# Kernel optimization log

Hardware: AMD Instinct MI355X
Metric: run time of the kernel (lower is better)

Reference implementation:

```python
import jax, jax.numpy as jnp
import numpy as np

# near_sym_b (13,19)-tap biorthogonal level-1 DTCWT filters (Kingsbury)
H0O = np.array([-0.0017578125, 0.0, 0.022265625, -0.046875, -0.0482421875,
                0.296875, 0.5554687500, 0.296875, -0.0482421875, -0.046875,
                0.022265625, 0.0, -0.0017578125], dtype=np.float32)
H1O = np.array([-7.0626e-05, 0.0, 1.34189e-03, -1.88341e-03, -7.15660e-03,
                2.38560e-02, 5.56431e-02, -5.16881e-02, -2.99758e-01,
                5.59431e-01, -2.99758e-01, -5.16881e-02, 5.56431e-02,
                2.38560e-02, -7.15660e-03, -1.88341e-03, 1.34189e-03,
                0.0, -7.0626e-05], dtype=np.float32)

def _alt(h):
    c = (len(h) - 1) // 2
    return (h * ((-1.0) ** (np.arange(len(h)) - c))).astype(np.float32)

G0O = _alt(H1O)  # synthesis lowpass  (PR complement of H1O)
G1O = _alt(H0O)  # synthesis highpass (PR complement of H0O)

DIM, HS, WS, BATCH, NB, BS = 64, 56, 56, 32, 4, 16


def _filt(x, h, axis):
    # depthwise 1D correlation with symmetric padding; x: (B,C,H,W), axis in {2,3}
    L = len(h); p = L // 2
    pad = [(0, 0)] * 4; pad[axis] = (p, p)
    xp = jnp.pad(x, pad, mode='symmetric')
    k = jnp.asarray(h, x.dtype).reshape((1, 1, L, 1) if axis == 2 else (1, 1, 1, L))
    B, C = x.shape[:2]
    y = jax.lax.conv_general_dilated(
        xp.reshape((B * C, 1) + xp.shape[2:]), k, (1, 1), 'VALID',
        dimension_numbers=('NCHW', 'OIHW', 'NCHW'))
    return y.reshape((B, C) + y.shape[2:])


def _q2c(y):
    y = y * np.float32(1.0 / np.sqrt(2.0))
    a = y[..., 0::2, 0::2]; b = y[..., 0::2, 1::2]
    c = y[..., 1::2, 0::2]; d = y[..., 1::2, 1::2]
    return (a - d, b + c), (a + d, b - c)


def _c2q(w1r, w1i, w2r, w2i):
    sc = np.float32(1.0 / np.sqrt(2.0))
    B, C, Hh, Wh = w1r.shape
    top = jnp.stack([(w1r + w2r) * sc, (w1i + w2i) * sc], axis=-1).reshape(B, C, Hh, 2 * Wh)
    bot = jnp.stack([(w1i - w2i) * sc, (w2r - w1r) * sc], axis=-1).reshape(B, C, Hh, 2 * Wh)
    return jnp.stack([top, bot], axis=3).reshape(B, C, 2 * Hh, 2 * Wh)


def dtcwt_fwd_j1(x):
    lo = _filt(x, H0O, 3); hi = _filt(x, H1O, 3)
    ll = _filt(lo, H0O, 2)
    (d15r, d15i), (d165r, d165i) = _q2c(_filt(lo, H1O, 2))   # LH -> 15/165 deg
    (d75r, d75i), (d105r, d105i) = _q2c(_filt(hi, H0O, 2))   # HL -> 75/105 deg
    (d45r, d45i), (d135r, d135i) = _q2c(_filt(hi, H1O, 2))   # HH -> 45/135 deg
    real = jnp.stack([d15r, d45r, d75r, d105r, d135r, d165r], axis=2)
    imag = jnp.stack([d15i, d45i, d75i, d105i, d135i, d165i], axis=2)
    return ll, jnp.stack([real, imag], axis=-1)  # (B,C,H,W), (B,C,6,H/2,W/2,2)


def dtcwt_inv_j1(ll, yh):
    r = yh[..., 0]; im = yh[..., 1]
    lh = _c2q(r[:, :, 0], im[:, :, 0], r[:, :, 5], im[:, :, 5])
    hl = _c2q(r[:, :, 2], im[:, :, 2], r[:, :, 3], im[:, :, 3])
    hh = _c2q(r[:, :, 1], im[:, :, 1], r[:, :, 4], im[:, :, 4])
    lo = _filt(ll, G0O, 2) + _filt(lh, G1O, 2)
    hi = _filt(hl, G0O, 2) + _filt(hh, G1O, 2)
    return _filt(lo, G0O, 3) + _filt(hi, G1O, 3)


def setup_inputs():
    key = jax.random.key(0)
    ks = jax.random.split(key, 6)
    return {
        'x': jax.random.normal(ks[0], (BATCH, HS * WS, DIM), jnp.float32),
        'w_ll': jax.random.normal(ks[1], (DIM, HS, WS), jnp.float32) * 0.02,
        'w1': jax.random.normal(ks[2], (2, NB, BS, BS), jnp.float32) * 0.02,
        'w2': jax.random.normal(ks[3], (2, NB, BS, BS), jnp.float32) * 0.02,
        'b1': jax.random.normal(ks[4], (2, NB, BS), jnp.float32) * 0.02,
        'b2': jax.random.normal(ks[5], (2, NB, BS), jnp.float32) * 0.02,
        'H': HS, 'W': WS,
    }


def reference(x, w_ll, w1, w2, b1, b2, H, W):
    Bt, N, C = x.shape
    xi = jnp.transpose(x.reshape(Bt, H, W, C), (0, 3, 1, 2)).astype(jnp.float32)
    xl, xh = dtcwt_fwd_j1(xi)
    xl = xl * w_ll                                  # (B,C,H,W) * (C,H,W)
    Hh, Wh = H // 2, W // 2
    # (B,C,6,Hh,Wh,2) -> (2,B,6,Hh,Wh,C) -> split C into (NB,BS) blocks
    xh = jnp.transpose(xh, (5, 0, 2, 3, 4, 1)).reshape(2, Bt, 6, Hh, Wh, NB, BS)
    xr, xim = xh[0], xh[1]
    mul = lambda t, w: jnp.einsum('...bd,bdk->...bk', t, w)
    r1 = jax.nn.relu(mul(xr, w1[0]) - mul(xim, w1[1]) + b1[0])
    i1 = jax.nn.relu(mul(xr, w1[1]) + mul(xim, w1[0]) + b1[1])
    r2 = mul(r1, w2[0]) - mul(i1, w2[1]) + b2[0]
    i2 = mul(r1, w2[1]) + mul(i1, w2[0]) + b2[1]
    xh2 = jnp.stack([r2, i2], axis=-1).reshape(Bt, 6, Hh, Wh, C, 2)
    xh2 = jnp.transpose(xh2, (0, 4, 1, 2, 3, 5))    # (B,C,6,Hh,Wh,2)
    y = dtcwt_inv_j1(xl, xh2)
    return jnp.transpose(y, (0, 2, 3, 1)).reshape(Bt, N, C)
```

## Files before the change

kernel.cpp:

```cpp
#include <hip/hip_runtime.h>

#define BT 32
#define CH 64
#define HS 56
#define WS 56
#define HH 28
#define WH 28

namespace {
constexpr float ISQ2 = 0.70710678118654752440f;
constexpr float F_H0[13] = {-0.0017578125f, 0.0f, 0.022265625f, -0.046875f,
    -0.0482421875f, 0.296875f, 0.55546875f, 0.296875f, -0.0482421875f,
    -0.046875f, 0.022265625f, 0.0f, -0.0017578125f};
constexpr float F_H1[19] = {-7.0626e-05f, 0.0f, 0.00134189f, -0.00188341f,
    -0.0071566f, 0.023856f, 0.0556431f, -0.0516881f, -0.299758f, 0.559431f,
    -0.299758f, -0.0516881f, 0.0556431f, 0.023856f, -0.0071566f,
    -0.00188341f, 0.00134189f, 0.0f, -7.0626e-05f};
constexpr float F_G0[19] = {7.0626e-05f, 0.0f, -0.00134189f, -0.00188341f,
    0.0071566f, 0.023856f, -0.0556431f, -0.0516881f, 0.299758f, 0.559431f,
    0.299758f, -0.0516881f, -0.0556431f, 0.023856f, 0.0071566f,
    -0.00188341f, -0.00134189f, 0.0f, 7.0626e-05f};
constexpr float F_G1[13] = {-0.0017578125f, 0.0f, 0.022265625f, 0.046875f,
    -0.0482421875f, -0.296875f, 0.55546875f, -0.296875f, -0.0482421875f,
    0.046875f, 0.022265625f, 0.0f, -0.0017578125f};
}

__device__ __forceinline__ int symi(int k) {
    k = (k < 0) ? (-1 - k) : k;
    k = (k >= HS) ? (2 * HS - 1 - k) : k;
    return k;
}

__device__ __forceinline__ unsigned short f2bf(float f) {
    unsigned u = __float_as_uint(f);
    u += 0x7fffu + ((u >> 16) & 1u);
    return (unsigned short)(u >> 16);
}
__device__ __forceinline__ float bf2f(unsigned short h) {
    return __uint_as_float(((unsigned)h) << 16);
}
__device__ __forceinline__ float2 bfp2(unsigned u) {
    float2 r;
    r.x = __uint_as_float((u & 0xffffu) << 16);
    r.y = __uint_as_float(u & 0xffff0000u);
    return r;
}
__device__ __forceinline__ unsigned packbf(float a, float b) {
    return (unsigned)f2bf(a) | ((unsigned)f2bf(b) << 16);
}

typedef __attribute__((ext_vector_type(8))) short short8;
typedef __attribute__((ext_vector_type(4))) float f32x4;

#define PPOS 784

__global__ __launch_bounds__(256) void k_fwd_rows(const float* __restrict__ x,
                                                  unsigned short* __restrict__ lo,
                                                  unsigned short* __restrict__ hi,
                                                  const float* __restrict__ wll,
                                                  float* __restrict__ wllT) {
    int b = blockIdx.x / HS, h = blockIdx.x % HS;
    int strip = threadIdx.x >> 5;
    int c0 = (threadIdx.x & 31) * 2;
    int base = (b * HS + h) * WS * CH + c0;
    const float* row = x + base;
    unsigned short* lop = lo + base;
    unsigned short* hip = hi + base;
    int w0s = strip * 7;
    float Wa[19], Wb[19];
#pragma unroll
    for (int t = 0; t < 19; ++t) {
        float2 v = *(const float2*)(row + symi(w0s - 9 + t) * CH);
        Wa[t] = v.x; Wb[t] = v.y;
    }
    float2 nW[7];
#pragma unroll
    for (int u = 0; u < 7; ++u) nW[u] = *(const float2*)(row + symi(w0s + u + 10) * CH);
#pragma unroll
    for (int u = 0; u < 7; ++u) {
        int w = w0s + u;
        float aLo = 0.f, aHi = 0.f, bLo = 0.f, bHi = 0.f;
#pragma unroll
        for (int t = 0; t < 13; ++t) { aLo += F_H0[t] * Wa[3 + t]; bLo += F_H0[t] * Wb[3 + t]; }
#pragma unroll
        for (int t = 0; t < 19; ++t) { aHi += F_H1[t] * Wa[t]; bHi += F_H1[t] * Wb[t]; }
        *(unsigned*)(lop + w * CH) = packbf(aLo, bLo);
        *(unsigned*)(hip + w * CH) = packbf(aHi, bHi);
#pragma unroll
        for (int t = 0; t < 18; ++t) { Wa[t] = Wa[t + 1]; Wb[t] = Wb[t + 1]; }
        Wa[18] = nW[u].x; Wb[18] = nW[u].y;
    }
    if (blockIdx.x < 49) {
        __shared__ float tile[64][65];
        int pos0 = blockIdx.x * 64;
        int lp = threadIdx.x & 63, g = threadIdx.x >> 6;
#pragma unroll
        for (int r = 0; r < 16; ++r) {
            int cc = r * 4 + g;
            tile[cc][lp] = wll[cc * (HS * WS) + pos0 + lp];
        }
        __syncthreads();
#pragma unroll
        for (int r = 0; r < 16; ++r) {
            int pl = r * 4 + g;
            wllT[(pos0 + pl) * CH + lp] = tile[lp][pl];
        }
    }
}

__global__ __launch_bounds__(256) void k_cols_mix(
    const unsigned short* __restrict__ lo_in,
    const unsigned short* __restrict__ hi_in, const float* __restrict__ wllT,
    const float* __restrict__ w1, const float* __restrict__ w2,
    const float* __restrict__ b1, const float* __restrict__ b2,
    unsigned short* __restrict__ xl, unsigned short* __restrict__ P0,
    unsigned short* __restrict__ P1, unsigned short* __restrict__ P2) {
    __shared__ __align__(16) unsigned short qTb[2][4][14][64];
    __shared__ __align__(16) unsigned short pA[8][14][72];
    unsigned short (*l1a)[16][36] =
        reinterpret_cast<unsigned short(*)[16][36]>(&qTb[0][0][0][0]);
    unsigned short (*l1b)[16][36] = l1a + 4;

    int hf = blockIdx.y;
    int zmode = blockIdx.z;
    int b = blockIdx.x / WH, wp = blockIdx.x % WH;
    int w0 = 2 * wp, tid = threadIdx.x;
    int q = tid >> 6, c = tid & 63;
    int rp = q >> 1, jc = q & 1;
    const unsigned short* srcp = zmode ? hi_in : lo_in;
    const unsigned short* colbase = srcp + (b * HS) * WS * CH + (w0 + jc) * CH + c;
    {
        int hstart = 2 * (hf * 14) + rp;
        float W[19];
#pragma unroll
        for (int t = 0; t < 19; ++t) W[t] = bf2f(colbase[symi(hstart - 9 + t) * (WS * CH)]);
        for (int rnd = 0; rnd < 2; ++rnd) {
            float nW0[7], nW1[7], nwll[7];
            int ii0 = rnd * 7;
#pragma unroll
            for (int u = 0; u < 7; ++u) {
                int h = hstart + 2 * (ii0 + u);
                nW0[u] = bf2f(colbase[symi(h + 10) * (WS * CH)]);
                nW1[u] = bf2f(colbase[symi(h + 11) * (WS * CH)]);
            }
            if (zmode == 0) {
#pragma unroll
                for (int u = 0; u < 7; ++u)
                    nwll[u] = wllT[((hstart + 2 * (ii0 + u)) * WS + (w0 + jc)) * CH + c];
            }
#pragma unroll
            for (int u = 0; u < 7; ++u) {
                int ii = ii0 + u;
                int h = hstart + 2 * ii;
                float v0 = 0.f, v1 = 0.f;
#pragma unroll
                for (int t = 0; t < 13; ++t) v0 += F_H0[t] * W[3 + t];
#pragma unroll
                for (int t = 0; t < 19; ++t) v1 += F_H1[t] * W[t];
                if (zmode == 0) {
                    xl[((b * HS + h) * WS + (w0 + jc)) * CH + c] = f2bf(v0 * nwll[u]);
                    qTb[0][q][ii][c] = f2bf(v1);
                } else {
                    qTb[0][q][ii][c] = f2bf(v0);
                    qTb[1][q][ii][c] = f2bf(v1);
                }
#pragma unroll
                for (int t = 0; t < 17; ++t) W[t] = W[t + 2];
                W[17] = nW0[u];
                W[18] = nW1[u];
            }
        }
    }
    __syncthreads();
    {
        int qq = tid >> 5;
        int role = qq & 3, half = qq >> 2;
        int c0 = (tid & 31) * 2;
        int rowA = role & 1, rowB = 3 - (role & 1);
        float sgn = (role == 1 || role == 2) ? 1.f : -1.f;
        if (zmode == 0) {
#pragma unroll
            for (int g = 0; g < 7; ++g) {
                int ii = half * 7 + g;
                float2 av = bfp2(*(const unsigned*)&qTb[0][rowA][ii][c0]);
                float2 bv = bfp2(*(const unsigned*)&qTb[0][rowB][ii][c0]);
                float v0 = (av.x + sgn * bv.x) * ISQ2;
                float v1 = (av.y + sgn * bv.y) * ISQ2;
                *(unsigned*)&pA[role][ii][c0] = packbf(v0, v1);
            }
        } else {
#pragma unroll
            for (int src = 0; src < 2; ++src) {
                int pl = (src == 0) ? (2 + role) : ((role < 2) ? role : (4 + role));
#pragma unroll
                for (int g = 0; g < 7; ++g) {
                    int ii = half * 7 + g;
                    float2 av = bfp2(*(const unsigned*)&qTb[src][rowA][ii][c0]);
                    float2 bv = bfp2(*(const unsigned*)&qTb[src][rowB][ii][c0]);
                    float v0 = (av.x + sgn * bv.x) * ISQ2;
                    float v1 = (av.y + sgn * bv.y) * ISQ2;
                    *(unsigned*)&pA[pl][ii][c0] = packbf(v0, v1);
                }
            }
        }
    }
    __syncthreads();

    int lane = tid & 63;
    int wv = tid >> 6;
    int nb = __builtin_amdgcn_readfirstlane(wv);
    int quad = lane >> 4;
    int n = lane & 15;
    int rix = quad >> 1, dlo = (quad & 1) * 8;
    int chb = nb * 16 + dlo;
    int npos = (n < 14) ? n : 0;

    short8 B1r, B1i, B2r, B2i;
#pragma unroll
    for (int j = 0; j < 8; ++j) {
        int kk = quad * 8 + j;
        int riw = kk >> 4, dd = kk & 15;
        float v1r = w1[nb * 256 + dd * 16 + n];
        float v1i = w1[1024 + nb * 256 + dd * 16 + n];
        float v2r = w2[nb * 256 + dd * 16 + n];
        float v2i = w2[1024 + nb * 256 + dd * 16 + n];
        B1r[j] = (short)f2bf(riw ? -v1i : v1r);
        B1i[j] = (short)f2bf(riw ? v1r : v1i);
        B2r[j] = (short)f2bf(riw ? -v2i : v2r);
        B2i[j] = (short)f2bf(riw ? v2r : v2i);
    }
    float bias1r = b1[nb * 16 + n], bias1i = b1[64 + nb * 16 + n];
    float bias2r = b2[nb * 16 + n], bias2i = b2[64 + nb * 16 + n];

    auto mixprod = [&](int aP, int bP, unsigned short* __restrict__ Pd) {
        short8 A1a = *(const short8*)&pA[aP][npos][chb];
        short8 A1b = *(const short8*)&pA[bP][npos][chb];
        f32x4 a1r = {bias1r, bias1r, bias1r, bias1r};
        f32x4 a1i = {bias1i, bias1i, bias1i, bias1i};
        f32x4 b1r_ = a1r, b1i_ = a1i;
        a1r = __builtin_amdgcn_mfma_f32_16x16x32_bf16(A1a, B1r, a1r, 0, 0, 0);
        a1i = __builtin_amdgcn_mfma_f32_16x16x32_bf16(A1a, B1i, a1i, 0, 0, 0);
        b1r_ = __builtin_amdgcn_mfma_f32_16x16x32_bf16(A1b, B1r, b1r_, 0, 0, 0);
        b1i_ = __builtin_amdgcn_mfma_f32_16x16x32_bf16(A1b, B1i, b1i_, 0, 0, 0);
#pragma unroll
        for (int r = 0; r < 4; ++r) {
            int pos = quad * 4 + r;
            l1a[wv][pos][n] = f2bf(fmaxf(a1r[r], 0.f));
            l1a[wv][pos][16 + n] = f2bf(fmaxf(a1i[r], 0.f));
            l1b[wv][pos][n] = f2bf(fmaxf(b1r_[r], 0.f));
            l1b[wv][pos][16 + n] = f2bf(fmaxf(b1i_[r], 0.f));
        }
        union { short8 s8; uint2 u2[2]; } a2a, a2b;
        const unsigned short* rowpa = &l1a[wv][n][0];
        const unsigned short* rowpb = &l1b[wv][n][0];
        a2a.u2[0] = *(const uint2*)(rowpa + quad * 8);
        a2a.u2[1] = *(const uint2*)(rowpa + quad * 8 + 4);
        a2b.u2[0] = *(const uint2*)(rowpb + quad * 8);
        a2b.u2[1] = *(const uint2*)(rowpb + quad * 8 + 4);
        f32x4 aAr = {bias2r, bias2r, bias2r, bias2r};
        f32x4 aAi = {bias2i, bias2i, bias2i, bias2i};
        f32x4 aBr = aAr, aBi = aAi;
        aAr = __builtin_amdgcn_mfma_f32_16x16x32_bf16(a2a.s8, B2r, aAr, 0, 0, 0);
        aAi = __builtin_amdgcn_mfma_f32_16x16x32_bf16(a2a.s8, B2i, aAi, 0, 0, 0);
        aBr = __builtin_amdgcn_mfma_f32_16x16x32_bf16(a2b.s8, B2r, aBr, 0, 0, 0);
        aBi = __builtin_amdgcn_mfma_f32_16x16x32_bf16(a2b.s8, B2i, aBi, 0, 0, 0);
#pragma unroll
        for (int r = 0; r < 4; ++r) {
            int m = quad * 4 + r;
            if (m < 14) {
                int iig = hf * 14 + m;
                int o = ((b * HS + 2 * iig) * WS + 2 * wp) * CH + nb * 16 + n;
                Pd[o] = f2bf((aAr[r] + aBr[r]) * ISQ2);
                Pd[o + CH] = f2bf((aAi[r] + aBi[r]) * ISQ2);
                Pd[o + WS * CH] = f2bf((aAi[r] - aBi[r]) * ISQ2);
                Pd[o + WS * CH + CH] = f2bf((aBr[r] - aAr[r]) * ISQ2);
            }
        }
    };

    if (zmode == 0) {
        mixprod(rix, 2 + rix, P0);
    } else {
        mixprod(2 + rix, 4 + rix, P1);
        mixprod(rix, 6 + rix, P2);
    }
}

template <int MODE>
__device__ __forceinline__ void inv_cols_body(
    const unsigned short* __restrict__ xl, const unsigned short* __restrict__ P0,
    const unsigned short* __restrict__ P1, const unsigned short* __restrict__ P2,
    unsigned short* __restrict__ lo2, unsigned short* __restrict__ hi2) {
    int hf = blockIdx.y;
    int b = blockIdx.x / 7, wg = blockIdx.x % 7;
    int wl = threadIdx.x >> 5, l = threadIdx.x & 31;
    int c0 = l * 2;
    int w = wg * 8 + wl;
    int base = (b * HS) * WS * CH + w * CH + c0;
    const int st = WS * CH;
    const unsigned short* Ap = (MODE == 0) ? xl : P1;
    const unsigned short* Bp = (MODE == 0) ? P0 : P2;
    unsigned short* outp = (MODE == 0) ? lo2 : hi2;
    auto ldA = [&](int r) -> float2 {
        return bfp2(*(const unsigned*)(Ap + base + r * st));
    };
    auto ldB = [&](int r) -> float2 {
        return bfp2(*(const unsigned*)(Bp + base + r * st));
    };
    int h0 = hf * 14;
    float Aa[19], Ab[19], Ba[13], Bb[13];
#pragma unroll
    for (int t = 0; t < 19; ++t) { float2 v = ldA(symi(h0 - 9 + t)); Aa[t] = v.x; Ab[t] = v.y; }
#pragma unroll
    for (int t = 0; t < 13; ++t) { float2 v = ldB(symi(h0 - 6 + t)); Ba[t] = v.x; Bb[t] = v.y; }
    float2 pa0[4], pb0[4], pa1[4], pb1[4];
#define LDG(bA, bB, OFF, CNT)                                                   \
    {                                                                           \
        _Pragma("unroll") for (int u = 0; u < (CNT); ++u)                       \
            bA[u] = ldA(symi(h0 + (OFF) + u + 10));                             \
        _Pragma("unroll") for (int u = 0; u < (CNT); ++u)                       \
            bB[u] = ldB(symi(h0 + (OFF) + u + 7));                              \
    }
#define CPG(bA, bB, OFF, CNT)                                                   \
    {                                                                           \
        _Pragma("unroll") for (int u = 0; u < (CNT); ++u) {                     \
            int h = h0 + (OFF) + u;                                             \
            float acca = 0.f, accb = 0.f;                                       \
            _Pragma("unroll") for (int t = 0; t < 19; ++t) {                    \
                acca += F_G0[t] * Aa[t]; accb += F_G0[t] * Ab[t];               \
            }                                                                   \
            _Pragma("unroll") for (int t = 0; t < 13; ++t) {                    \
                acca += F_G1[t] * Ba[t]; accb += F_G1[t] * Bb[t];               \
            }                                                                   \
            *(unsigned*)(outp + base + h * st) = packbf(acca, accb);            \
            _Pragma("unroll") for (int t = 0; t < 18; ++t) {                    \
                Aa[t] = Aa[t + 1]; Ab[t] = Ab[t + 1];                           \
            }                                                                   \
            _Pragma("unroll") for (int t = 0; t < 12; ++t) {                    \
                Ba[t] = Ba[t + 1]; Bb[t] = Bb[t + 1];                           \
            }                                                                   \
            Aa[18] = bA[u].x; Ab[18] = bA[u].y;                                 \
            Ba[12] = bB[u].x; Bb[12] = bB[u].y;                                 \
        }                                                                       \
    }
    LDG(pa0, pb0, 0, 4) LDG(pa1, pb1, 4, 4)
    CPG(pa0, pb0, 0, 4) LDG(pa0, pb0, 8, 4)
    CPG(pa1, pb1, 4, 4) LDG(pa1, pb1, 12, 2)
    CPG(pa0, pb0, 8, 4)
    CPG(pa1, pb1, 12, 2)
#undef LDG
#undef CPG
}

__global__ __launch_bounds__(256) void k_inv_cols(
    const unsigned short* __restrict__ xl, const unsigned short* __restrict__ P0,
    const unsigned short* __restrict__ P1, const unsigned short* __restrict__ P2,
    unsigned short* __restrict__ lo2, unsigned short* __restrict__ hi2) {
    if (blockIdx.z == 0)
        inv_cols_body<0>(xl, P0, P1, P2, lo2, hi2);
    else
        inv_cols_body<1>(xl, P0, P1, P2, lo2, hi2);
}

__global__ __launch_bounds__(256) void k_inv_rows(
    const unsigned short* __restrict__ lo2,
    const unsigned short* __restrict__ hi2, float* __restrict__ out) {
    int b = blockIdx.x / HS, h = blockIdx.x % HS;
    int strip = threadIdx.x >> 5;
    int c0 = (threadIdx.x & 31) * 2;
    int base = (b * HS + h) * WS * CH + c0;
    const unsigned short* rlo = lo2 + base;
    const unsigned short* rhi = hi2 + base;
    float* op = out + base;
    int w0s = strip * 7;
    float Aa[19], Ab[19], Ba[13], Bb[13];
#pragma unroll
    for (int t = 0; t < 19; ++t) {
        float2 v = bfp2(*(const unsigned*)(rlo + symi(w0s - 9 + t) * CH));
        Aa[t] = v.x; Ab[t] = v.y;
    }
#pragma unroll
    for (int t = 0; t < 13; ++t) {
        float2 v = bfp2(*(const unsigned*)(rhi + symi(w0s - 6 + t) * CH));
        Ba[t] = v.x; Bb[t] = v.y;
    }
    float2 nA[7], nB[7];
#pragma unroll
    for (int u = 0; u < 7; ++u) nA[u] = bfp2(*(const unsigned*)(rlo + symi(w0s + u + 10) * CH));
#pragma unroll
    for (int u = 0; u < 7; ++u) nB[u] = bfp2(*(const unsigned*)(rhi + symi(w0s + u + 7) * CH));
#pragma unroll
    for (int u = 0; u < 7; ++u) {
        int w = w0s + u;
        float acca = 0.f, accb = 0.f;
#pragma unroll
        for (int t = 0; t < 19; ++t) { acca += F_G0[t] * Aa[t]; accb += F_G0[t] * Ab[t]; }
#pragma unroll
        for (int t = 0; t < 13; ++t) { acca += F_G1[t] * Ba[t]; accb += F_G1[t] * Bb[t]; }
        float2 ov; ov.x = acca; ov.y = accb;
        *(float2*)(op + w * CH) = ov;
#pragma unroll
        for (int t = 0; t < 18; ++t) { Aa[t] = Aa[t + 1]; Ab[t] = Ab[t + 1]; }
#pragma unroll
        for (int t = 0; t < 12; ++t) { Ba[t] = Ba[t + 1]; Bb[t] = Bb[t + 1]; }
        Aa[18] = nA[u].x; Ab[18] = nA[u].y;
        Ba[12] = nB[u].x; Bb[12] = nB[u].y;
    }
}

extern "C" void kernel_launch(void* const* d_in, const int* in_sizes, int n_in,
                              void* d_out, int out_size, void* d_ws, size_t ws_size,
                              hipStream_t stream) {
    const float* x = (const float*)d_in[0];
    const float* w_ll = (const float*)d_in[1];
    const float* w1 = (const float*)d_in[2];
    const float* w2 = (const float*)d_in[3];
    const float* b1 = (const float*)d_in[4];
    const float* b2 = (const float*)d_in[5];
    float* out = (float*)d_out;

    const size_t A = (size_t)BT * HS * WS * CH;
    const size_t SBf = (size_t)12 * 64 * BT * PPOS / 2;
    float* wsf = (float*)d_ws;
    unsigned short* xl = (unsigned short*)wsf;
    unsigned short* lo2 = (unsigned short*)(wsf + A);
    unsigned short* hi2 = (unsigned short*)(wsf + A + SBf);
    unsigned short* lo_in = (unsigned short*)(wsf + A + SBf + A);
    unsigned short* hi_in = lo_in + A;
    unsigned short* P0 = hi_in + A;
    unsigned short* P1 = P0 + A;
    unsigned short* P2 = P1 + A;

    float* wllT = out;

    k_fwd_rows<<<BT * HS, 256, 0, stream>>>(x, lo_in, hi_in, w_ll, wllT);
    k_cols_mix<<<dim3(BT * WH, 2, 2), 256, 0, stream>>>(lo_in, hi_in, wllT, w1,
                                                        w2, b1, b2, xl, P0, P1, P2);
    k_inv_cols<<<dim3(BT * 7, 4, 2), 256, 0, stream>>>(xl, P0, P1, P2, lo2, hi2);
    k_inv_rows<<<BT * HS, 256, 0, stream>>>(lo2, hi2, out);
}
```

Before: 162.8 us.

## Specialize cols_mix on mode/half, ring-buffer window, packed bf16 cvt, precompute weights

Templates the column/mix kernel on z-mode and half index so symmetric-boundary handling applies only on the side that needs it. It replaces the shifting filter window with an indexed ring buffer and uses v_cvt_pk_bf16_f32 for paired bf16 conversions. The bf16 MFMA weight fragments are now built once by a spare block of the forward-rows kernel and stored in a workspace slot, rather than recomputed in every cols_mix block. This trims address math, register moves and conversion instructions, at the cost of more code size and a dependency on the workspace layout.

```diff
diff --git a/kernel.cpp b/kernel.cpp
--- a/kernel.cpp
+++ b/kernel.cpp
@@ -30,6 +30,8 @@
     k = (k >= HS) ? (2 * HS - 1 - k) : k;
     return k;
 }
+__device__ __forceinline__ int symi_lo(int k) { return (k < 0) ? (-1 - k) : k; }
+__device__ __forceinline__ int symi_hi(int k) { return (k >= HS) ? (2 * HS - 1 - k) : k; }
 
 __device__ __forceinline__ unsigned short f2bf(float f) {
     unsigned u = __float_as_uint(f);
@@ -38,6 +40,11 @@
 }
 __device__ __forceinline__ float bf2f(unsigned short h) {
     return __uint_as_float(((unsigned)h) << 16);
+}
+__device__ __forceinline__ unsigned cvtpk(float lo, float hi) {
+    unsigned r;
+    asm("v_cvt_pk_bf16_f32 %0, %1, %2" : "=v"(r) : "v"(lo), "v"(hi));
+    return r;
 }
 __device__ __forceinline__ float2 bfp2(unsigned u) {
     float2 r;
@@ -58,7 +65,10 @@
                                                   unsigned short* __restrict__ lo,
                                                   unsigned short* __restrict__ hi,
                                                   const float* __restrict__ wll,
-                                                  float* __restrict__ wllT) {
+                                                  float* __restrict__ wllT,
+                                                  const float* __restrict__ w1,
+                                                  const float* __restrict__ w2,
+                                                  unsigned short* __restrict__ wB) {
     int b = blockIdx.x / HS, h = blockIdx.x % HS;
     int strip = threadIdx.x >> 5;
     int c0 = (threadIdx.x & 31) * 2;
@@ -105,69 +115,96 @@
             int pl = r * 4 + g;
             wllT[(pos0 + pl) * CH + lp] = tile[lp][pl];
         }
-    }
-}
-
-__global__ __launch_bounds__(256) void k_cols_mix(
+    } else if (blockIdx.x == 49) {
+        int tid = threadIdx.x;
+        int lane = tid & 63;
+        int nb = tid >> 6;
+        int quad = lane >> 4, n = lane & 15;
+        short8 B1r, B1i, B2r, B2i;
+#pragma unroll
+        for (int j = 0; j < 8; ++j) {
+            int kk = quad * 8 + j;
+            int riw = kk >> 4, dd = kk & 15;
+            float v1r = w1[nb * 256 + dd * 16 + n];
+            float v1i = w1[1024 + nb * 256 + dd * 16 + n];
+            float v2r = w2[nb * 256 + dd * 16 + n];
+            float v2i = w2[1024 + nb * 256 + dd * 16 + n];
+            B1r[j] = (short)f2bf(riw ? -v1i : v1r);
+            B1i[j] = (short)f2bf(riw ? v1r : v1i);
+            B2r[j] = (short)f2bf(riw ? -v2i : v2r);
+            B2i[j] = (short)f2bf(riw ? v2r : v2i);
+        }
+        *(short8*)(wB + (0 * 256 + tid) * 8) = B1r;
+        *(short8*)(wB + (1 * 256 + tid) * 8) = B1i;
+        *(short8*)(wB + (2 * 256 + tid) * 8) = B2r;
+        *(short8*)(wB + (3 * 256 + tid) * 8) = B2i;
+    }
+}
+
+template <int ZM, int HF>
+__device__ __forceinline__ void cols_mix_body(
+    unsigned short (&qTb)[2][4][14][64], unsigned short (&pA)[8][14][72],
     const unsigned short* __restrict__ lo_in,
     const unsigned short* __restrict__ hi_in, const float* __restrict__ wllT,
-    const float* __restrict__ w1, const float* __restrict__ w2,
-    const float* __restrict__ b1, const float* __restrict__ b2,
-    unsigned short* __restrict__ xl, unsigned short* __restrict__ P0,
-    unsigned short* __restrict__ P1, unsigned short* __restrict__ P2) {
-    __shared__ __align__(16) unsigned short qTb[2][4][14][64];
-    __shared__ __align__(16) unsigned short pA[8][14][72];
+    const unsigned short* __restrict__ wB, const float* __restrict__ b1,
+    const float* __restrict__ b2, unsigned short* __restrict__ xl,
+    unsigned short* __restrict__ P0, unsigned short* __restrict__ P1,
+    unsigned short* __restrict__ P2) {
     unsigned short (*l1a)[16][36] =
         reinterpret_cast<unsigned short(*)[16][36]>(&qTb[0][0][0][0]);
     unsigned short (*l1b)[16][36] = l1a + 4;
 
-    int hf = blockIdx.y;
-    int zmode = blockIdx.z;
     int b = blockIdx.x / WH, wp = blockIdx.x % WH;
     int w0 = 2 * wp, tid = threadIdx.x;
     int q = tid >> 6, c = tid & 63;
     int rp = q >> 1, jc = q & 1;
-    const unsigned short* srcp = zmode ? hi_in : lo_in;
+    const unsigned short* srcp = ZM ? hi_in : lo_in;
     const unsigned short* colbase = srcp + (b * HS) * WS * CH + (w0 + jc) * CH + c;
     {
-        int hstart = 2 * (hf * 14) + rp;
+        int hstart = HF * 28 + rp;
         float W[19];
 #pragma unroll
-        for (int t = 0; t < 19; ++t) W[t] = bf2f(colbase[symi(hstart - 9 + t) * (WS * CH)]);
+        for (int t = 0; t < 19; ++t) {
+            int r = (HF == 0) ? symi_lo(hstart - 9 + t) : (hstart - 9 + t);
+            W[t] = bf2f(colbase[r * (WS * CH)]);
+        }
+#pragma unroll
         for (int rnd = 0; rnd < 2; ++rnd) {
             float nW0[7], nW1[7], nwll[7];
             int ii0 = rnd * 7;
 #pragma unroll
             for (int u = 0; u < 7; ++u) {
                 int h = hstart + 2 * (ii0 + u);
-                nW0[u] = bf2f(colbase[symi(h + 10) * (WS * CH)]);
-                nW1[u] = bf2f(colbase[symi(h + 11) * (WS * CH)]);
-            }
-            if (zmode == 0) {
+                int r0 = (HF == 0) ? (h + 10) : symi_hi(h + 10);
+                int r1 = (HF == 0) ? (h + 11) : symi_hi(h + 11);
+                nW0[u] = bf2f(colbase[r0 * (WS * CH)]);
+                nW1[u] = bf2f(colbase[r1 * (WS * CH)]);
+            }
+            if (ZM == 0) {
 #pragma unroll
                 for (int u = 0; u < 7; ++u)
                     nwll[u] = wllT[((hstart + 2 * (ii0 + u)) * WS + (w0 + jc)) * CH + c];
             }
 #pragma unroll
             for (int u = 0; u < 7; ++u) {
-                int ii = ii0 + u;
+                const int ii = ii0 + u;
                 int h = hstart + 2 * ii;
                 float v0 = 0.f, v1 = 0.f;
 #pragma unroll
-                for (int t = 0; t < 13; ++t) v0 += F_H0[t] * W[3 + t];
-#pragma unroll
-                for (int t = 0; t < 19; ++t) v1 += F_H1[t] * W[t];
-                if (zmode == 0) {
-                    xl[((b * HS + h) * WS + (w0 + jc)) * CH + c] = f2bf(v0 * nwll[u]);
-                    qTb[0][q][ii][c] = f2bf(v1);
+                for (int t = 0; t < 13; ++t) v0 += F_H0[t] * W[(2 * ii + 3 + t) % 19];
+#pragma unroll
+                for (int t = 0; t < 19; ++t) v1 += F_H1[t] * W[(2 * ii + t) % 19];
+                if (ZM == 0) {
+                    unsigned pk = cvtpk(v0 * nwll[u], v1);
+                    xl[((b * HS + h) * WS + (w0 + jc)) * CH + c] = (unsigned short)pk;
+                    qTb[0][q][ii][c] = (unsigned short)(pk >> 16);
                 } else {
-                    qTb[0][q][ii][c] = f2bf(v0);
-                    qTb[1][q][ii][c] = f2bf(v1);
+                    unsigned pk = cvtpk(v0, v1);
+                    qTb[0][q][ii][c] = (unsigned short)pk;
+                    qTb[1][q][ii][c] = (unsigned short)(pk >> 16);
                 }
-#pragma unroll
-                for (int t = 0; t < 17; ++t) W[t] = W[t + 2];
-                W[17] = nW0[u];
-                W[18] = nW1[u];
+                W[(2 * ii) % 19] = nW0[u];
+                W[(2 * ii + 1) % 19] = nW1[u];
             }
         }
     }
@@ -178,15 +215,14 @@
         int c0 = (tid & 31) * 2;
         int rowA = role & 1, rowB = 3 - (role & 1);
         float sgn = (role == 1 || role == 2) ? 1.f : -1.f;
-        if (zmode == 0) {
+        if (ZM == 0) {
 #pragma unroll
             for (int g = 0; g < 7; ++g) {
                 int ii = half * 7 + g;
                 float2 av = bfp2(*(const unsigned*)&qTb[0][rowA][ii][c0]);
                 float2 bv = bfp2(*(const unsigned*)&qTb[0][rowB][ii][c0]);
-                float v0 = (av.x + sgn * bv.x) * ISQ2;
-                float v1 = (av.y + sgn * bv.y) * ISQ2;
-                *(unsigned*)&pA[role][ii][c0] = packbf(v0, v1);
+                *(unsigned*)&pA[role][ii][c0] =
+                    cvtpk((av.x + sgn * bv.x) * ISQ2, (av.y + sgn * bv.y) * ISQ2);
             }
         } else {
 #pragma unroll
@@ -197,9 +233,8 @@
                     int ii = half * 7 + g;
                     float2 av = bfp2(*(const unsigned*)&qTb[src][rowA][ii][c0]);
                     float2 bv = bfp2(*(const unsigned*)&qTb[src][rowB][ii][c0]);
-                    float v0 = (av.x + sgn * bv.x) * ISQ2;
-                    float v1 = (av.y + sgn * bv.y) * ISQ2;
-                    *(unsigned*)&pA[pl][ii][c0] = packbf(v0, v1);
+                    *(unsigned*)&pA[pl][ii][c0] =
+                        cvtpk((av.x + sgn * bv.x) * ISQ2, (av.y + sgn * bv.y) * ISQ2);
                 }
             }
         }
@@ -215,20 +250,10 @@
     int chb = nb * 16 + dlo;
     int npos = (n < 14) ? n : 0;
 
-    short8 B1r, B1i, B2r, B2i;
-#pragma unroll
-    for (int j = 0; j < 8; ++j) {
-        int kk = quad * 8 + j;
-        int riw = kk >> 4, dd = kk & 15;
-        float v1r = w1[nb * 256 + dd * 16 + n];
-        float v1i = w1[1024 + nb * 256 + dd * 16 + n];
-        float v2r = w2[nb * 256 + dd * 16 + n];
-        float v2i = w2[1024 + nb * 256 + dd * 16 + n];
-        B1r[j] = (short)f2bf(riw ? -v1i : v1r);
-        B1i[j] = (short)f2bf(riw ? v1r : v1i);
-        B2r[j] = (short)f2bf(riw ? -v2i : v2r);
-        B2i[j] = (short)f2bf(riw ? v2r : v2i);
-    }
+    short8 B1r = *(const short8*)(wB + (0 * 256 + tid) * 8);
+    short8 B1i = *(const short8*)(wB + (1 * 256 + tid) * 8);
+    short8 B2r = *(const short8*)(wB + (2 * 256 + tid) * 8);
+    short8 B2i = *(const short8*)(wB + (3 * 256 + tid) * 8);
     float bias1r = b1[nb * 16 + n], bias1i = b1[64 + nb * 16 + n];
     float bias2r = b2[nb * 16 + n], bias2i = b2[64 + nb * 16 + n];
 
@@ -245,10 +270,12 @@
 #pragma unroll
         for (int r = 0; r < 4; ++r) {
             int pos = quad * 4 + r;
-            l1a[wv][pos][n] = f2bf(fmaxf(a1r[r], 0.f));
-            l1a[wv][pos][16 + n] = f2bf(fmaxf(a1i[r], 0.f));
-            l1b[wv][pos][n] = f2bf(fmaxf(b1r_[r], 0.f));
-            l1b[wv][pos][16 + n] = f2bf(fmaxf(b1i_[r], 0.f));
+            unsigned pka = cvtpk(fmaxf(a1r[r], 0.f), fmaxf(a1i[r], 0.f));
+            unsigned pkb = cvtpk(fmaxf(b1r_[r], 0.f), fmaxf(b1i_[r], 0.f));
+            l1a[wv][pos][n] = (unsigned short)pka;
+            l1a[wv][pos][16 + n] = (unsigned short)(pka >> 16);
+            l1b[wv][pos][n] = (unsigned short)pkb;
+            l1b[wv][pos][16 + n] = (unsigned short)(pkb >> 16);
         }
         union { short8 s8; uint2 u2[2]; } a2a, a2b;
         const unsigned short* rowpa = &l1a[wv][n][0];
@@ -268,21 +295,45 @@
         for (int r = 0; r < 4; ++r) {
             int m = quad * 4 + r;
             if (m < 14) {
-                int iig = hf * 14 + m;
+                int iig = HF * 14 + m;
                 int o = ((b * HS + 2 * iig) * WS + 2 * wp) * CH + nb * 16 + n;
-                Pd[o] = f2bf((aAr[r] + aBr[r]) * ISQ2);
-                Pd[o + CH] = f2bf((aAi[r] + aBi[r]) * ISQ2);
-                Pd[o + WS * CH] = f2bf((aAi[r] - aBi[r]) * ISQ2);
-                Pd[o + WS * CH + CH] = f2bf((aBr[r] - aAr[r]) * ISQ2);
+                unsigned pk0 = cvtpk((aAr[r] + aBr[r]) * ISQ2, (aAi[r] + aBi[r]) * ISQ2);
+                unsigned pk1 = cvtpk((aAi[r] - aBi[r]) * ISQ2, (aBr[r] - aAr[r]) * ISQ2);
+                Pd[o] = (unsigned short)pk0;
+                Pd[o + CH] = (unsigned short)(pk0 >> 16);
+                Pd[o + WS * CH] = (unsigned short)pk1;
+                Pd[o + WS * CH + CH] = (unsigned short)(pk1 >> 16);
             }
         }
     };
 
-    if (zmode == 0) {
+    if (ZM == 0) {
         mixprod(rix, 2 + rix, P0);
     } else {
         mixprod(2 + rix, 4 + rix, P1);
         mixprod(rix, 6 + rix, P2);
+    }
+}
+
+__global__ __launch_bounds__(256) void k_cols_mix(
+    const unsigned short* __restrict__ lo_in,
+    const unsigned short* __restrict__ hi_in, const float* __restrict__ wllT,
+    const unsigned short* __restrict__ wB, const float* __restrict__ b1,
+    const float* __restrict__ b2, unsigned short* __restrict__ xl,
+    unsigned short* __restrict__ P0, unsigned short* __restrict__ P1,
+    unsigned short* __restrict__ P2) {
+    __shared__ __align__(16) unsigned short qTb[2][4][14][64];
+    __shared__ __align__(16) unsigned short pA[8][14][72];
+    if (blockIdx.z == 0) {
+        if (blockIdx.y == 0)
+            cols_mix_body<0, 0>(qTb, pA, lo_in, hi_in, wllT, wB, b1, b2, xl, P0, P1, P2);
+        else
+            cols_mix_body<0, 1>(qTb, pA, lo_in, hi_in, wllT, wB, b1, b2, xl, P0, P1, P2);
+    } else {
+        if (blockIdx.y == 0)
+            cols_mix_body<1, 0>(qTb, pA, lo_in, hi_in, wllT, wB, b1, b2, xl, P0, P1, P2);
+        else
+            cols_mix_body<1, 1>(qTb, pA, lo_in, hi_in, wllT, wB, b1, b2, xl, P0, P1, P2);
     }
 }
 
@@ -425,6 +476,7 @@
     unsigned short* xl = (unsigned short*)wsf;
     unsigned short* lo2 = (unsigned short*)(wsf + A);
     unsigned short* hi2 = (unsigned short*)(wsf + A + SBf);
+    unsigned short* wB = (unsigned short*)(wsf + A + SBf + A / 2);
     unsigned short* lo_in = (unsigned short*)(wsf + A + SBf + A);
     unsigned short* hi_in = lo_in + A;
     unsigned short* P0 = hi_in + A;
@@ -433,9 +485,9 @@
 
     float* wllT = out;
 
-    k_fwd_rows<<<BT * HS, 256, 0, stream>>>(x, lo_in, hi_in, w_ll, wllT);
-    k_cols_mix<<<dim3(BT * WH, 2, 2), 256, 0, stream>>>(lo_in, hi_in, wllT, w1,
-                                                        w2, b1, b2, xl, P0, P1, P2);
+    k_fwd_rows<<<BT * HS, 256, 0, stream>>>(x, lo_in, hi_in, w_ll, wllT, w1, w2, wB);
+    k_cols_mix<<<dim3(BT * WH, 2, 2), 256, 0, stream>>>(lo_in, hi_in, wllT, wB,
+                                                        b1, b2, xl, P0, P1, P2);
     k_inv_cols<<<dim3(BT * 7, 4, 2), 256, 0, stream>>>(xl, P0, P1, P2, lo2, hi2);
     k_inv_rows<<<BT * HS, 256, 0, stream>>>(lo2, hi2, out);
 }
```

Result: faster. 149.9 us (-7.9%).
